# Kernel optimization log

Hardware: AMD Instinct MI355X
Metric: run time of the kernel (lower is better)

Reference implementation:

```python
import jax, jax.numpy as jnp
import numpy as np

EMBED_DIM = 1024
NUM_HEADS = 16


def setup_inputs() -> dict:
    key = jax.random.key(0)
    kq, kk, kv = jax.random.split(key, 3)
    N, L, S, E = 4, 2048, 2048, EMBED_DIM
    return {
        "query": jax.random.normal(kq, (N, L, E), dtype=jnp.float32),
        "key": jax.random.normal(kk, (N, S, E), dtype=jnp.float32),
        "value": jax.random.normal(kv, (N, S, E), dtype=jnp.float32),
        "is_causal": 1,
    }


def reference(query, key, value, is_causal):
    N, L, E = query.shape
    _, S, E_v = value.shape
    H = NUM_HEADS
    dh = E // H
    dh_v = E_v // H
    # (N, H, L, dh) layout
    q = query.reshape(N, L, H, dh).transpose(0, 2, 1, 3)
    k = key.reshape(N, S, H, dh).transpose(0, 2, 1, 3)
    v = value.reshape(N, S, H, dh_v).transpose(0, 2, 1, 3)

    scale = 1.0 / np.sqrt(dh).astype(np.float32)
    # full LxS score matrix, as in the original (non-flash)
    scores = jnp.einsum('nhld,nhsd->nhls', q, k) * scale
    if is_causal:
        causal = jnp.tril(jnp.ones((L, S), dtype=bool))  # True = allowed
        scores = jnp.where(causal, scores, jnp.float32(-jnp.inf))
    attn_weight = jax.nn.softmax(scores, axis=-1)  # (N,H,L,S)
    y = jnp.einsum('nhls,nhsd->nhld', attn_weight, v)
    y = y.transpose(0, 2, 1, 3).reshape(N, L, E_v)
    return (y, attn_weight)
```

## Files before the change

### kernel.cpp

```cpp
#include <hip/hip_runtime.h>
#include <math.h>
#include <stdint.h>

#define N_B 4
#define N_H 16
#define L_Q 2048
#define L_K 2048
#define E_D 1024
#define DH  64
#define QB  128
#define KB  64
#define NT  512
#define NQT (L_Q / QB)
#define NKT (L_K / KB)
#define LDP  72
#define LDPV 68

typedef _Float16 f16x2 __attribute__((ext_vector_type(2)));
typedef _Float16 f16x4 __attribute__((ext_vector_type(4)));
typedef _Float16 f16x8 __attribute__((ext_vector_type(8)));
typedef float    f32x4 __attribute__((ext_vector_type(4)));

__device__ __forceinline__ f16x4 pk4(float a, float b, float c, float d) {
    f16x2 lo = __builtin_bit_cast(f16x2, __builtin_amdgcn_cvt_pkrtz(a, b));
    f16x2 hi = __builtin_bit_cast(f16x2, __builtin_amdgcn_cvt_pkrtz(c, d));
    f16x4 r; r[0] = lo[0]; r[1] = lo[1]; r[2] = hi[0]; r[3] = hi[1];
    return r;
}

__device__ __forceinline__ f16x8 pk8(float4 a, float4 b) {
    f16x4 lo = pk4(a.x, a.y, a.z, a.w);
    f16x4 hi = pk4(b.x, b.y, b.z, b.w);
    return __builtin_shufflevector(lo, hi, 0, 1, 2, 3, 4, 5, 6, 7);
}

__device__ __forceinline__ void gload16(const _Float16* g, _Float16* l) {
    __builtin_amdgcn_global_load_lds(
        (const __attribute__((address_space(1))) void*)g,
        (__attribute__((address_space(3))) void*)l, 16, 0, 0);
}

__global__ __launch_bounds__(256)
void cvt_k(const float* __restrict__ K, _Float16* __restrict__ Kh)
{
    size_t i = ((size_t)blockIdx.x * 256 + threadIdx.x) * 8;
    float4 c = *(const float4*)(K + i);
    float4 d = *(const float4*)(K + i + 4);
    *(f16x4*)(Kh + i)     = pk4(c.x, c.y, c.z, c.w);
    *(f16x4*)(Kh + i + 4) = pk4(d.x, d.y, d.z, d.w);
}

__global__ __launch_bounds__(256)
void cvt_vt(const float* __restrict__ V, _Float16* __restrict__ Vt)
{
    __shared__ _Float16 T[64][72];
    const int bid = blockIdx.x;
    const int st  = bid & 31;
    const int nh  = bid >> 5;
    const int n   = nh >> 4;
    const int h   = nh & 15;
    const int t   = threadIdx.x;
    const float* Vb = V + ((size_t)(n * L_K + st * 64)) * E_D + h * DH;
    #pragma unroll
    for (int i = 0; i < 4; ++i) {
        int lin = t + i * 256;
        int s = lin >> 4, d = (lin & 15) * 4;
        float4 v = *(const float4*)(Vb + (size_t)s * E_D + d);
        T[d + 0][s] = (_Float16)v.x; T[d + 1][s] = (_Float16)v.y;
        T[d + 2][s] = (_Float16)v.z; T[d + 3][s] = (_Float16)v.w;
    }
    __syncthreads();
    _Float16* Ob = Vt + ((size_t)nh * DH) * L_K + st * 64;
    #pragma unroll
    for (int j = 0; j < 2; ++j) {
        int lin = t + j * 256;
        int d = lin >> 3, sc = (lin & 7) * 8;
        *(f16x8*)(Ob + (size_t)d * L_K + sc) = *(const f16x8*)&T[d][sc];
    }
}

__global__ __launch_bounds__(NT)
void mha_main(const float* __restrict__ Qg, const _Float16* __restrict__ Kh,
              const _Float16* __restrict__ Vth, const int* __restrict__ causp,
              float* __restrict__ Yg, float* __restrict__ Wg)
{
    __shared__ __attribute__((aligned(16))) _Float16 KsL[2][KB * DH];
    __shared__ __attribute__((aligned(16))) _Float16 VsL[2][DH * KB];
    __shared__ __attribute__((aligned(16))) _Float16 Ps[QB][LDP];
    __shared__ float linv[QB];

    const int tid  = threadIdx.x;
    const int lane = tid & 63;
    const int wid  = tid >> 6;
    const int bid0 = blockIdx.x;
    const int bid  = ((bid0 & 7) << 7) + (bid0 >> 3);
    const int qt   = (NQT - 1) - (bid & (NQT - 1));
    const int nh   = bid >> 4;
    const int q0   = qt * QB;
    const int n    = nh >> 4;
    const int h    = nh & 15;
    const bool causal = (*causp) != 0;
    const float scale = 0.125f;

    const int lrow = lane & 15;
    const int g    = lane >> 4;
    const int rb   = wid * 16;
    const int rsub = g * 4;
    const int kt_end = causal ? (2 * qt + 2) : NKT;

    float*  Ybase = Yg + ((size_t)(n * L_Q + q0)) * E_D + h * DH;
    float*  Wbase = Wg + ((size_t)nh * L_Q + q0) * L_K;

    const int srow = wid * 8 + (lane >> 3);
    const int scol = (((lane & 7) ^ ((lane >> 3) & 7)) << 3);
    const _Float16* Ksrc0 = Kh  + ((size_t)(n * L_K) + srow) * E_D + h * DH + scol;
    const _Float16* Vsrc0 = Vth + ((size_t)nh * DH + srow) * L_K + scol;

    const int swz = (lrow & 7) << 4;
    const int cb0 = ((g * 16) ^ swz) >> 1;
    const int cb1 = ((64 + g * 16) ^ swz) >> 1;

    const float* Qrowf = Qg + ((size_t)(n * L_Q + q0 + rb + lrow)) * E_D + h * DH;
    const f16x8 qf0 = pk8(*(const float4*)(Qrowf + g * 8),
                          *(const float4*)(Qrowf + g * 8 + 4));
    const f16x8 qf1 = pk8(*(const float4*)(Qrowf + 32 + g * 8),
                          *(const float4*)(Qrowf + 32 + g * 8 + 4));

    #define STAGE_K(b, kt) gload16(Ksrc0 + (size_t)(kt) * KB * E_D, &KsL[b][wid * 512])
    #define STAGE_KV(b, kt) gload16(Ksrc0 + (size_t)(kt) * KB * E_D, &VsL[b][wid * 512])
    #define STAGE_V(b, kt) gload16(Vsrc0 + (size_t)(kt) * KB,       &VsL[b][wid * 512])
    #define FRAG(buf, tc, half) (*(const f16x8*)&(buf)[(size_t)((tc) * 16 + lrow) * 64 + ((half) ? cb1 : cb0)])

    float l_part = 0.0f;
    {
        const int np = kt_end >> 1;
        STAGE_K(0, 0);
        STAGE_KV(0, 1);
        for (int p = 0; p < np; ++p) {
            __builtin_amdgcn_sched_barrier(0);
            asm volatile("s_waitcnt vmcnt(0) lgkmcnt(0)" ::: "memory");
            __builtin_amdgcn_s_barrier();
            __builtin_amdgcn_sched_barrier(0);
            if (p + 1 < np) {
                STAGE_K((p + 1) & 1, 2 * p + 2);
                STAGE_KV((p + 1) & 1, 2 * p + 3);
            }
            #pragma unroll
            for (int half = 0; half < 2; ++half) {
                const int kt = 2 * p + half;
                const _Float16* Kc = half ? &VsL[p & 1][0] : &KsL[p & 1][0];
                f32x4 acc[4] = {};
                #pragma unroll
                for (int tc = 0; tc < 4; ++tc) {
                    acc[tc] = __builtin_amdgcn_mfma_f32_16x16x32_f16(FRAG(Kc, tc, 0), qf0, acc[tc], 0, 0, 0);
                    acc[tc] = __builtin_amdgcn_mfma_f32_16x16x32_f16(FRAG(Kc, tc, 1), qf1, acc[tc], 0, 0, 0);
                }
                const bool dm = causal && (kt >= 2 * qt);
                const int krel = (kt - 2 * qt) * 64;
                #pragma unroll
                for (int tc = 0; tc < 4; ++tc) {
                    #pragma unroll
                    for (int i = 0; i < 4; ++i) {
                        float v = acc[tc][i] * scale;
                        bool ok = !dm || (krel + tc * 16 + rsub + i <= rb + lrow);
                        l_part += ok ? __expf(v) : 0.0f;
                    }
                }
            }
        }
        __syncthreads();
    }
    l_part += __shfl_xor(l_part, 16);
    l_part += __shfl_xor(l_part, 32);
    const float inv_l = 1.0f / l_part;
    linv[rb + lrow] = inv_l;

    f32x4 o[4] = {};
    STAGE_K(0, 0);
    STAGE_V(0, 0);
    __syncthreads();

    float winv[4];
    #pragma unroll
    for (int j = 0; j < 4; ++j) winv[j] = linv[rb + (lane >> 4) + 4 * j];

    for (int kt = 0; kt < kt_end; ++kt) {
        const int cur = kt & 1;
        if (kt + 1 < kt_end) { STAGE_K(cur ^ 1, kt + 1); STAGE_V(cur ^ 1, kt + 1); }

        f32x4 acc[4] = {};
        #pragma unroll
        for (int tc = 0; tc < 4; ++tc) {
            acc[tc] = __builtin_amdgcn_mfma_f32_16x16x32_f16(FRAG(KsL[cur], tc, 0), qf0, acc[tc], 0, 0, 0);
            acc[tc] = __builtin_amdgcn_mfma_f32_16x16x32_f16(FRAG(KsL[cur], tc, 1), qf1, acc[tc], 0, 0, 0);
        }

        const bool dm = causal && (kt >= 2 * qt);
        const int krel = (kt - 2 * qt) * 64;
        #pragma unroll
        for (int tc = 0; tc < 4; ++tc) {
            float v, p0, p1, p2, p3;
            v = acc[tc][0] * scale;
            p0 = (!dm || (krel + tc * 16 + rsub + 0 <= rb + lrow)) ? __expf(v) : 0.0f;
            v = acc[tc][1] * scale;
            p1 = (!dm || (krel + tc * 16 + rsub + 1 <= rb + lrow)) ? __expf(v) : 0.0f;
            v = acc[tc][2] * scale;
            p2 = (!dm || (krel + tc * 16 + rsub + 2 <= rb + lrow)) ? __expf(v) : 0.0f;
            v = acc[tc][3] * scale;
            p3 = (!dm || (krel + tc * 16 + rsub + 3 <= rb + lrow)) ? __expf(v) : 0.0f;
            *(f16x4*)&Ps[rb + lrow][tc * 16 + rsub] = pk4(p0, p1, p2, p3);
        }

        f16x8 pf0 = *(const f16x8*)&Ps[rb + lrow][0 + g * 8];
        f16x8 pf1 = *(const f16x8*)&Ps[rb + lrow][32 + g * 8];
        #pragma unroll
        for (int tc = 0; tc < 4; ++tc) {
            o[tc] = __builtin_amdgcn_mfma_f32_16x16x32_f16(FRAG(VsL[cur], tc, 0), pf0, o[tc], 0, 0, 0);
            o[tc] = __builtin_amdgcn_mfma_f32_16x16x32_f16(FRAG(VsL[cur], tc, 1), pf1, o[tc], 0, 0, 0);
        }

        {
            float* Wt = Wbase + (size_t)kt * KB;
            const int c0 = (lane & 15) * 4;
            #pragma unroll
            for (int j = 0; j < 4; ++j) {
                const int rl = rb + (lane >> 4) + 4 * j;
                f16x4 pv = *(const f16x4*)&Ps[rl][c0];
                const float s = winv[j];
                f32x4 wv = { (float)pv[0] * s, (float)pv[1] * s,
                             (float)pv[2] * s, (float)pv[3] * s };
                __builtin_nontemporal_store(wv, (f32x4*)(Wt + (size_t)rl * L_K + c0));
            }
        }

        __builtin_amdgcn_sched_barrier(0);
        asm volatile("s_waitcnt vmcnt(4) lgkmcnt(0)" ::: "memory");
        __builtin_amdgcn_s_barrier();
        __builtin_amdgcn_sched_barrier(0);
    }

    #pragma unroll
    for (int tc = 0; tc < 4; ++tc) {
        f32x4 yv = { o[tc][0] * inv_l, o[tc][1] * inv_l,
                     o[tc][2] * inv_l, o[tc][3] * inv_l };
        __builtin_nontemporal_store(yv, (f32x4*)(Ybase + (size_t)(rb + lrow) * E_D + tc * 16 + rsub));
    }

    if (causal && kt_end < NKT) {
        const int c0 = kt_end * KB;
        const int rem4 = (L_K - c0) >> 2;
        const f32x4 z = { 0.f, 0.f, 0.f, 0.f };
        for (int r = 0; r < QB; ++r) {
            float* row = Wbase + (size_t)r * L_K + c0;
            for (int c4 = tid; c4 < rem4; c4 += NT) {
                __builtin_nontemporal_store(z, (f32x4*)(row + c4 * 4));
            }
        }
    }
    #undef STAGE_K
    #undef STAGE_KV
    #undef STAGE_V
    #undef FRAG
}

__global__ __launch_bounds__(256)
void mha_fwd_fallback(const float* __restrict__ Qg, const float* __restrict__ Kg,
                      const float* __restrict__ Vg, const int* __restrict__ causp,
                      float* __restrict__ Yg, float* __restrict__ Wg)
{
    __shared__ __attribute__((aligned(16))) _Float16 Qs[64][LDP];
    __shared__ __attribute__((aligned(16))) _Float16 Ks[64][LDP];
    __shared__ __attribute__((aligned(16))) _Float16 Psf[64][LDP];
    __shared__ __attribute__((aligned(16))) _Float16 Vt[DH][LDPV];

    const int tid  = threadIdx.x;
    const int lane = tid & 63;
    const int wid  = tid >> 6;
    const int bid  = blockIdx.x;
    const int qt   = bid & 31;
    const int nh   = bid >> 5;
    const int q0   = qt * 64;
    const int n    = nh >> 4;
    const int h    = nh & 15;
    const bool causal = (*causp) != 0;
    const float scale = 0.125f;

    const float* Qbase = Qg + ((size_t)(n * L_Q + q0)) * E_D + h * DH;
    const float* Kbase = Kg + ((size_t)n * L_K) * E_D + h * DH;
    const float* Vbase = Vg + ((size_t)n * L_K) * E_D + h * DH;
    float*       Ybase = Yg + ((size_t)(n * L_Q + q0)) * E_D + h * DH;
    float*       Wbase = Wg + ((size_t)nh * L_Q + q0) * L_K;

    const int lrow = lane & 15;
    const int lk   = (lane >> 4) * 8;
    const int rb   = wid * 16;
    const int rsub = (lane >> 4) * 4;
    const int kt_end = causal ? (qt + 1) : NKT;

    #pragma unroll
    for (int i = 0; i < 4; ++i) {
        int lin = tid + i * 256;
        int r = lin >> 4;
        int c = (lin & 15) * 4;
        float4 qv = *(const float4*)(Qbase + (size_t)r * E_D + c);
        *(f16x4*)&Qs[r][c] = pk4(qv.x, qv.y, qv.z, qv.w);
    }
    __syncthreads();
    const f16x8 qf0 = *(const f16x8*)&Qs[rb + lrow][lk];
    const f16x8 qf1 = *(const f16x8*)&Qs[rb + lrow][32 + lk];

    float l_part = 0.0f;
    for (int kt = 0; kt < kt_end; ++kt) {
        const float* Kt = Kbase + (size_t)kt * KB * E_D;
        __syncthreads();
        #pragma unroll
        for (int i = 0; i < 4; ++i) {
            int lin = tid + i * 256;
            int r = lin >> 4;
            int c = (lin & 15) * 4;
            float4 kv = *(const float4*)(Kt + (size_t)r * E_D + c);
            *(f16x4*)&Ks[r][c] = pk4(kv.x, kv.y, kv.z, kv.w);
        }
        __syncthreads();
        f32x4 acc[4] = {};
        #pragma unroll
        for (int tc = 0; tc < 4; ++tc) {
            f16x8 a0 = *(const f16x8*)&Ks[tc * 16 + lrow][lk];
            f16x8 a1 = *(const f16x8*)&Ks[tc * 16 + lrow][32 + lk];
            acc[tc] = __builtin_amdgcn_mfma_f32_16x16x32_f16(a0, qf0, acc[tc], 0, 0, 0);
            acc[tc] = __builtin_amdgcn_mfma_f32_16x16x32_f16(a1, qf1, acc[tc], 0, 0, 0);
        }
        const bool dm = causal && (kt == qt);
        #pragma unroll
        for (int tc = 0; tc < 4; ++tc) {
            #pragma unroll
            for (int i = 0; i < 4; ++i) {
                float v = acc[tc][i] * scale;
                bool ok = !dm || (tc * 16 + rsub + i <= rb + lrow);
                l_part += ok ? __expf(v) : 0.0f;
            }
        }
    }
    l_part += __shfl_xor(l_part, 16);
    l_part += __shfl_xor(l_part, 32);
    const float inv_l = 1.0f / l_part;

    f32x4 o[4] = {};
    for (int kt = 0; kt < kt_end; ++kt) {
        const float* Kt  = Kbase + (size_t)kt * KB * E_D;
        const float* Vtg = Vbase + (size_t)kt * KB * E_D;
        __syncthreads();
        #pragma unroll
        for (int i = 0; i < 4; ++i) {
            int lin = tid + i * 256;
            int r = lin >> 4;
            int c = (lin & 15) * 4;
            float4 kv = *(const float4*)(Kt + (size_t)r * E_D + c);
            *(f16x4*)&Ks[r][c] = pk4(kv.x, kv.y, kv.z, kv.w);
            int d   = lin & 63;
            int kk0 = (lin >> 6) * 4;
            float v0 = Vtg[(size_t)(kk0 + 0) * E_D + d];
            float v1 = Vtg[(size_t)(kk0 + 1) * E_D + d];
            float v2 = Vtg[(size_t)(kk0 + 2) * E_D + d];
            float v3 = Vtg[(size_t)(kk0 + 3) * E_D + d];
            *(f16x4*)&Vt[d][kk0] = pk4(v0, v1, v2, v3);
        }
        __syncthreads();
        f32x4 acc[4] = {};
        #pragma unroll
        for (int tc = 0; tc < 4; ++tc) {
            f16x8 a0 = *(const f16x8*)&Ks[tc * 16 + lrow][lk];
            f16x8 a1 = *(const f16x8*)&Ks[tc * 16 + lrow][32 + lk];
            acc[tc] = __builtin_amdgcn_mfma_f32_16x16x32_f16(a0, qf0, acc[tc], 0, 0, 0);
            acc[tc] = __builtin_amdgcn_mfma_f32_16x16x32_f16(a1, qf1, acc[tc], 0, 0, 0);
        }
        const bool dm = causal && (kt == qt);
        float* Wrow = Wbase + (size_t)(rb + lrow) * L_K + kt * KB;
        #pragma unroll
        for (int tc = 0; tc < 4; ++tc) {
            float v, p0, p1, p2, p3;
            v = acc[tc][0] * scale;
            p0 = (!dm || (tc * 16 + rsub + 0 <= rb + lrow)) ? __expf(v) : 0.0f;
            v = acc[tc][1] * scale;
            p1 = (!dm || (tc * 16 + rsub + 1 <= rb + lrow)) ? __expf(v) : 0.0f;
            v = acc[tc][2] * scale;
            p2 = (!dm || (tc * 16 + rsub + 2 <= rb + lrow)) ? __expf(v) : 0.0f;
            v = acc[tc][3] * scale;
            p3 = (!dm || (tc * 16 + rsub + 3 <= rb + lrow)) ? __expf(v) : 0.0f;
            float4 wv = make_float4(p0 * inv_l, p1 * inv_l, p2 * inv_l, p3 * inv_l);
            *(float4*)(Wrow + tc * 16 + rsub) = wv;
            *(f16x4*)&Psf[rb + lrow][tc * 16 + rsub] = pk4(p0, p1, p2, p3);
        }
        f16x8 pf0 = *(const f16x8*)&Psf[rb + lrow][lk];
        f16x8 pf1 = *(const f16x8*)&Psf[rb + lrow][32 + lk];
        #pragma unroll
        for (int tc = 0; tc < 4; ++tc) {
            f16x4 t0 = *(const f16x4*)&Vt[tc * 16 + lrow][lk];
            f16x4 t1 = *(const f16x4*)&Vt[tc * 16 + lrow][lk + 4];
            f16x8 a0 = __builtin_shufflevector(t0, t1, 0, 1, 2, 3, 4, 5, 6, 7);
            f16x4 t2 = *(const f16x4*)&Vt[tc * 16 + lrow][32 + lk];
            f16x4 t3 = *(const f16x4*)&Vt[tc * 16 + lrow][32 + lk + 4];
            f16x8 a1 = __builtin_shufflevector(t2, t3, 0, 1, 2, 3, 4, 5, 6, 7);
            o[tc] = __builtin_amdgcn_mfma_f32_16x16x32_f16(a0, pf0, o[tc], 0, 0, 0);
            o[tc] = __builtin_amdgcn_mfma_f32_16x16x32_f16(a1, pf1, o[tc], 0, 0, 0);
        }
    }
    #pragma unroll
    for (int tc = 0; tc < 4; ++tc) {
        float4 yv = make_float4(o[tc][0] * inv_l, o[tc][1] * inv_l,
                                o[tc][2] * inv_l, o[tc][3] * inv_l);
        *(float4*)(Ybase + (size_t)(rb + lrow) * E_D + tc * 16 + rsub) = yv;
    }
    if (causal && kt_end < NKT) {
        const int c0 = kt_end * KB;
        const int rem4 = (L_K - c0) >> 2;
        const float4 z = make_float4(0.f, 0.f, 0.f, 0.f);
        for (int r = 0; r < 64; ++r) {
            float* row = Wbase + (size_t)r * L_K + c0;
            for (int c4 = tid; c4 < rem4; c4 += 256) {
                *(float4*)(row + c4 * 4) = z;
            }
        }
    }
}

extern "C" void kernel_launch(void* const* d_in, const int* in_sizes, int n_in,
                              void* d_out, int out_size, void* d_ws, size_t ws_size,
                              hipStream_t stream) {
    const float* Q  = (const float*)d_in[0];
    const float* K  = (const float*)d_in[1];
    const float* V  = (const float*)d_in[2];
    const int* caus = (const int*)d_in[3];
    float* Y = (float*)d_out;
    float* W = (float*)d_out + (size_t)N_B * L_Q * E_D;

    const size_t elems = (size_t)N_B * L_Q * E_D;
    const size_t need  = 2 * elems * sizeof(_Float16);

    if (ws_size >= need) {
        _Float16* Kh = (_Float16*)d_ws;
        _Float16* Vt = Kh + elems;
        hipLaunchKernelGGL(cvt_k, dim3(elems / (256 * 8)), dim3(256), 0, stream, K, Kh);
        hipLaunchKernelGGL(cvt_vt, dim3(N_B * N_H * (L_K / 64)), dim3(256), 0, stream, V, Vt);
        hipLaunchKernelGGL(mha_main, dim3(N_B * N_H * NQT), dim3(NT), 0, stream,
                           Q, Kh, Vt, caus, Y, W);
    } else {
        hipLaunchKernelGGL(mha_fwd_fallback, dim3(N_B * N_H * 32), dim3(256), 0, stream,
                           Q, K, V, caus, Y, W);
    }
}
```

Baseline: 269.5 us.

## Triple-buffer K tiles in softmax-sum pass and merge K/V conversion kernels

Replaces the separate K/V/P shared arrays with one unified shared buffer. The first pass (row-sum of exponentials over K) now uses a three-slot ring with prefetch two pairs ahead and a partial vmcnt wait, so global-to-LDS loads overlap compute instead of draining each iteration. The K conversion and V transpose kernels are fused into a single launch, dispatched by block index, to save one kernel launch. The deeper ring needs 3×8192 halves of LDS, and the fixed waitcnt value depends on exactly two loads per stage.

```diff
diff --git a/kernel.cpp b/kernel.cpp
--- a/kernel.cpp
+++ b/kernel.cpp
@@ -14,7 +14,7 @@
 #define NQT (L_Q / QB)
 #define NKT (L_K / KB)
 #define LDP  72
-#define LDPV 68
+#define TILE 4096
 
 typedef _Float16 f16x2 __attribute__((ext_vector_type(2)));
 typedef _Float16 f16x4 __attribute__((ext_vector_type(4)));
@@ -41,25 +41,25 @@
 }
 
 __global__ __launch_bounds__(256)
-void cvt_k(const float* __restrict__ K, _Float16* __restrict__ Kh)
-{
-    size_t i = ((size_t)blockIdx.x * 256 + threadIdx.x) * 8;
-    float4 c = *(const float4*)(K + i);
-    float4 d = *(const float4*)(K + i + 4);
-    *(f16x4*)(Kh + i)     = pk4(c.x, c.y, c.z, c.w);
-    *(f16x4*)(Kh + i + 4) = pk4(d.x, d.y, d.z, d.w);
-}
-
-__global__ __launch_bounds__(256)
-void cvt_vt(const float* __restrict__ V, _Float16* __restrict__ Vt)
+void cvt_kv(const float* __restrict__ K, const float* __restrict__ V,
+            _Float16* __restrict__ Kh, _Float16* __restrict__ Vt)
 {
     __shared__ _Float16 T[64][72];
-    const int bid = blockIdx.x;
+    const int b = blockIdx.x;
+    const int t = threadIdx.x;
+    if (b < 4096) {
+        size_t i = ((size_t)b * 256 + t) * 8;
+        float4 c = *(const float4*)(K + i);
+        float4 d = *(const float4*)(K + i + 4);
+        *(f16x4*)(Kh + i)     = pk4(c.x, c.y, c.z, c.w);
+        *(f16x4*)(Kh + i + 4) = pk4(d.x, d.y, d.z, d.w);
+        return;
+    }
+    const int bid = b - 4096;
     const int st  = bid & 31;
     const int nh  = bid >> 5;
     const int n   = nh >> 4;
     const int h   = nh & 15;
-    const int t   = threadIdx.x;
     const float* Vb = V + ((size_t)(n * L_K + st * 64)) * E_D + h * DH;
     #pragma unroll
     for (int i = 0; i < 4; ++i) {
@@ -84,9 +84,7 @@
               const _Float16* __restrict__ Vth, const int* __restrict__ causp,
               float* __restrict__ Yg, float* __restrict__ Wg)
 {
-    __shared__ __attribute__((aligned(16))) _Float16 KsL[2][KB * DH];
-    __shared__ __attribute__((aligned(16))) _Float16 VsL[2][DH * KB];
-    __shared__ __attribute__((aligned(16))) _Float16 Ps[QB][LDP];
+    __shared__ __attribute__((aligned(16))) _Float16 SM[25600];
     __shared__ float linv[QB];
 
     const int tid  = threadIdx.x;
@@ -126,29 +124,41 @@
     const f16x8 qf1 = pk8(*(const float4*)(Qrowf + 32 + g * 8),
                           *(const float4*)(Qrowf + 32 + g * 8 + 4));
 
-    #define STAGE_K(b, kt) gload16(Ksrc0 + (size_t)(kt) * KB * E_D, &KsL[b][wid * 512])
-    #define STAGE_KV(b, kt) gload16(Ksrc0 + (size_t)(kt) * KB * E_D, &VsL[b][wid * 512])
-    #define STAGE_V(b, kt) gload16(Vsrc0 + (size_t)(kt) * KB,       &VsL[b][wid * 512])
+    #define KSL(b)    (SM + (b) * TILE)
+    #define VSL(b)    (SM + (2 + (b)) * TILE)
+    #define PS_ROW(r) (SM + 4 * TILE + (size_t)(r) * LDP)
     #define FRAG(buf, tc, half) (*(const f16x8*)&(buf)[(size_t)((tc) * 16 + lrow) * 64 + ((half) ? cb1 : cb0)])
 
     float l_part = 0.0f;
     {
         const int np = kt_end >> 1;
-        STAGE_K(0, 0);
-        STAGE_KV(0, 1);
+        gload16(Ksrc0 + (size_t)0 * KB * E_D, SM + 0 * 8192 + wid * 512);
+        gload16(Ksrc0 + (size_t)1 * KB * E_D, SM + 0 * 8192 + TILE + wid * 512);
+        if (np > 1) {
+            gload16(Ksrc0 + (size_t)2 * KB * E_D, SM + 1 * 8192 + wid * 512);
+            gload16(Ksrc0 + (size_t)3 * KB * E_D, SM + 1 * 8192 + TILE + wid * 512);
+        }
+        int slot = 0;
         for (int p = 0; p < np; ++p) {
             __builtin_amdgcn_sched_barrier(0);
-            asm volatile("s_waitcnt vmcnt(0) lgkmcnt(0)" ::: "memory");
+            if (p + 1 < np) {
+                asm volatile("s_waitcnt vmcnt(2) lgkmcnt(0)" ::: "memory");
+            } else {
+                asm volatile("s_waitcnt vmcnt(0) lgkmcnt(0)" ::: "memory");
+            }
             __builtin_amdgcn_s_barrier();
             __builtin_amdgcn_sched_barrier(0);
-            if (p + 1 < np) {
-                STAGE_K((p + 1) & 1, 2 * p + 2);
-                STAGE_KV((p + 1) & 1, 2 * p + 3);
-            }
+            if (p + 2 < np) {
+                int ns = slot + 2; if (ns >= 3) ns -= 3;
+                gload16(Ksrc0 + (size_t)(2 * p + 4) * KB * E_D, SM + ns * 8192 + wid * 512);
+                gload16(Ksrc0 + (size_t)(2 * p + 5) * KB * E_D, SM + ns * 8192 + TILE + wid * 512);
+            }
+            __builtin_amdgcn_sched_barrier(0);
+            const _Float16* base = SM + slot * 8192;
             #pragma unroll
             for (int half = 0; half < 2; ++half) {
                 const int kt = 2 * p + half;
-                const _Float16* Kc = half ? &VsL[p & 1][0] : &KsL[p & 1][0];
+                const _Float16* Kc = base + half * TILE;
                 f32x4 acc[4] = {};
                 #pragma unroll
                 for (int tc = 0; tc < 4; ++tc) {
@@ -167,6 +177,7 @@
                     }
                 }
             }
+            slot = slot + 1; if (slot >= 3) slot = 0;
         }
         __syncthreads();
     }
@@ -176,8 +187,8 @@
     linv[rb + lrow] = inv_l;
 
     f32x4 o[4] = {};
-    STAGE_K(0, 0);
-    STAGE_V(0, 0);
+    gload16(Ksrc0, KSL(0) + wid * 512);
+    gload16(Vsrc0, VSL(0) + wid * 512);
     __syncthreads();
 
     float winv[4];
@@ -186,13 +197,16 @@
 
     for (int kt = 0; kt < kt_end; ++kt) {
         const int cur = kt & 1;
-        if (kt + 1 < kt_end) { STAGE_K(cur ^ 1, kt + 1); STAGE_V(cur ^ 1, kt + 1); }
+        if (kt + 1 < kt_end) {
+            gload16(Ksrc0 + (size_t)(kt + 1) * KB * E_D, KSL(cur ^ 1) + wid * 512);
+            gload16(Vsrc0 + (size_t)(kt + 1) * KB,       VSL(cur ^ 1) + wid * 512);
+        }
 
         f32x4 acc[4] = {};
         #pragma unroll
         for (int tc = 0; tc < 4; ++tc) {
-            acc[tc] = __builtin_amdgcn_mfma_f32_16x16x32_f16(FRAG(KsL[cur], tc, 0), qf0, acc[tc], 0, 0, 0);
-            acc[tc] = __builtin_amdgcn_mfma_f32_16x16x32_f16(FRAG(KsL[cur], tc, 1), qf1, acc[tc], 0, 0, 0);
+            acc[tc] = __builtin_amdgcn_mfma_f32_16x16x32_f16(FRAG(KSL(cur), tc, 0), qf0, acc[tc], 0, 0, 0);
+            acc[tc] = __builtin_amdgcn_mfma_f32_16x16x32_f16(FRAG(KSL(cur), tc, 1), qf1, acc[tc], 0, 0, 0);
         }
 
         const bool dm = causal && (kt >= 2 * qt);
@@ -208,15 +222,15 @@
             p2 = (!dm || (krel + tc * 16 + rsub + 2 <= rb + lrow)) ? __expf(v) : 0.0f;
             v = acc[tc][3] * scale;
             p3 = (!dm || (krel + tc * 16 + rsub + 3 <= rb + lrow)) ? __expf(v) : 0.0f;
-            *(f16x4*)&Ps[rb + lrow][tc * 16 + rsub] = pk4(p0, p1, p2, p3);
-        }
-
-        f16x8 pf0 = *(const f16x8*)&Ps[rb + lrow][0 + g * 8];
-        f16x8 pf1 = *(const f16x8*)&Ps[rb + lrow][32 + g * 8];
-        #pragma unroll
-        for (int tc = 0; tc < 4; ++tc) {
-            o[tc] = __builtin_amdgcn_mfma_f32_16x16x32_f16(FRAG(VsL[cur], tc, 0), pf0, o[tc], 0, 0, 0);
-            o[tc] = __builtin_amdgcn_mfma_f32_16x16x32_f16(FRAG(VsL[cur], tc, 1), pf1, o[tc], 0, 0, 0);
+            *(f16x4*)(PS_ROW(rb + lrow) + tc * 16 + rsub) = pk4(p0, p1, p2, p3);
+        }
+
+        f16x8 pf0 = *(const f16x8*)(PS_ROW(rb + lrow) + g * 8);
+        f16x8 pf1 = *(const f16x8*)(PS_ROW(rb + lrow) + 32 + g * 8);
+        #pragma unroll
+        for (int tc = 0; tc < 4; ++tc) {
+            o[tc] = __builtin_amdgcn_mfma_f32_16x16x32_f16(FRAG(VSL(cur), tc, 0), pf0, o[tc], 0, 0, 0);
+            o[tc] = __builtin_amdgcn_mfma_f32_16x16x32_f16(FRAG(VSL(cur), tc, 1), pf1, o[tc], 0, 0, 0);
         }
 
         {
@@ -225,7 +239,7 @@
             #pragma unroll
             for (int j = 0; j < 4; ++j) {
                 const int rl = rb + (lane >> 4) + 4 * j;
-                f16x4 pv = *(const f16x4*)&Ps[rl][c0];
+                f16x4 pv = *(const f16x4*)(PS_ROW(rl) + c0);
                 const float s = winv[j];
                 f32x4 wv = { (float)pv[0] * s, (float)pv[1] * s,
                              (float)pv[2] * s, (float)pv[3] * s };
@@ -257,9 +271,9 @@
             }
         }
     }
-    #undef STAGE_K
-    #undef STAGE_KV
-    #undef STAGE_V
+    #undef KSL
+    #undef VSL
+    #undef PS_ROW
     #undef FRAG
 }
 
@@ -271,7 +285,7 @@
     __shared__ __attribute__((aligned(16))) _Float16 Qs[64][LDP];
     __shared__ __attribute__((aligned(16))) _Float16 Ks[64][LDP];
     __shared__ __attribute__((aligned(16))) _Float16 Psf[64][LDP];
-    __shared__ __attribute__((aligned(16))) _Float16 Vt[DH][LDPV];
+    __shared__ __attribute__((aligned(16))) _Float16 Vt[DH][68];
 
     const int tid  = threadIdx.x;
     const int lane = tid & 63;
@@ -440,8 +454,8 @@
     if (ws_size >= need) {
         _Float16* Kh = (_Float16*)d_ws;
         _Float16* Vt = Kh + elems;
-        hipLaunchKernelGGL(cvt_k, dim3(elems / (256 * 8)), dim3(256), 0, stream, K, Kh);
-        hipLaunchKernelGGL(cvt_vt, dim3(N_B * N_H * (L_K / 64)), dim3(256), 0, stream, V, Vt);
+        hipLaunchKernelGGL(cvt_kv, dim3(4096 + N_B * N_H * (L_K / 64)), dim3(256), 0, stream,
+                           K, V, Kh, Vt);
         hipLaunchKernelGGL(mha_main, dim3(N_B * N_H * NQT), dim3(NT), 0, stream,
                            Q, Kh, Vt, caus, Y, W);
     } else {
```

After: 266.4 us, median of 2. About the same (-1.2%).
